# Optimization experiments

Hardware: AMD Instinct MI355X
Metric: run time of the kernel (lower is better)

The kernel has to match this reference:

```python
import jax, jax.numpy as jnp
import numpy as np

NP, NA, H, K, TAU = 4096, 2048, 128, 5, 1.0
NODE_N = {'paper': NP, 'author': NA}
RELS = [('pp', 'paper', 'paper'), ('aa', 'author', 'author'),
        ('pa', 'paper', 'author'), ('ap', 'author', 'paper')]


def setup_inputs():
    key = jax.random.key(0)
    ks = jax.random.split(key, 32)
    f32 = jnp.float32
    def nrm(k, shape, scale=1.0):
        return jax.random.normal(k, shape, f32) * scale
    Epp, Eaa, Epa, Eap = 131072, 65536, 131072, 131072
    inp = {
        'x_paper': nrm(ks[0], (NP, H)),
        'x_author': nrm(ks[1], (NA, H)),
        'ei_pp': jax.random.randint(ks[2], (2, Epp), 0, NP, dtype=jnp.int32),
        'ei_aa': jax.random.randint(ks[3], (2, Eaa), 0, NA, dtype=jnp.int32),
        'ei_pa': jnp.stack([jax.random.randint(ks[4], (Epa,), 0, NP, dtype=jnp.int32),
                            jax.random.randint(ks[5], (Epa,), 0, NA, dtype=jnp.int32)]),
        'ei_ap': jnp.stack([jax.random.randint(ks[6], (Eap,), 0, NA, dtype=jnp.int32),
                            jax.random.randint(ks[7], (Eap,), 0, NP, dtype=jnp.int32)]),
        'batch_paper': jnp.zeros((NP,), jnp.int32),
        'batch_author': jnp.zeros((NA,), jnp.int32),
        'index': 7,
    }
    s = H ** -0.5
    i = 8
    for t in ('paper', 'author'):
        for l in (0, 1):
            inp['Wself_%s%d' % (t, l)] = nrm(ks[i], (H, H), s); i += 1
    for r, _, _ in RELS:
        for l in (0, 1):
            inp['W%s%d' % (r, l)] = nrm(ks[i], (H, H), s); i += 1
    for r in ('pp', 'aa'):
        inp['Wep1_%s' % r] = nrm(ks[i], (2 * H, 256), (2 * H) ** -0.5); i += 1
        inp['bep1_%s' % r] = jnp.zeros((256,), f32)
        inp['Wep2_%s' % r] = nrm(ks[i], (256, 2), 256 ** -0.5); i += 1
        inp['bep2_%s' % r] = jnp.zeros((2,), f32)
    inp['Wc'] = nrm(ks[i], (H, 5), s)
    inp['bc'] = jnp.zeros((5,), f32)
    return inp


def _mean_agg(msg, dst, n):
    s = jax.ops.segment_sum(msg, dst, num_segments=n)
    c = jax.ops.segment_sum(jnp.ones((msg.shape[0], 1), msg.dtype), dst, num_segments=n)
    return s / jnp.maximum(c, 1.0)


def _gnn(x, ei, p, single, edge_attn=None):
    # 2-layer relation-typed mean-aggregation hetero GNN.
    h = dict(x)
    for l in (0, 1):
        nh = {}
        for t in ('paper', 'author'):
            agg = h[t] @ p['Wself_%s%d' % (t, l)]
            for r, s_t, d_t in RELS:
                if d_t != t or (single and s_t != d_t):
                    continue
                src, dst = ei[r][0], ei[r][1]
                msg = h[s_t][src] @ p['W%s%d' % (r, l)]  # [E, H]
                if edge_attn is not None and r in edge_attn:
                    msg = msg * edge_attn[r][:, None]
                agg = agg + _mean_agg(msg, dst, NODE_N[t])
            nh[t] = jax.nn.relu(agg)
        h = nh
    return h


def _edge_pred(h, ei, p, r, t):
    src, dst = ei[r][0], ei[r][1]
    e = jnp.concatenate([h[t][src], h[t][dst]], axis=-1)  # [E, 2H]
    e = jax.nn.relu(e @ p['Wep1_%s' % r] + p['bep1_%s' % r])
    return e @ p['Wep2_%s' % r] + p['bep2_%s' % r]  # [E, 2]


def _gumbel_topk(logits, mask, k, tau, key):
    # Masked straight-through top-k gumbel-softmax (row-wise, hard=True).
    u = jax.random.uniform(key, logits.shape, logits.dtype, 1e-10, 1.0)
    g = -jnp.log(-jnp.log(u))
    y = jnp.where(mask, (logits + g) / tau, -1e9)
    soft = jax.nn.softmax(y, axis=-1)
    _, idx = jax.lax.top_k(soft, k)  # [N, k]
    rows = jnp.arange(logits.shape[0])[:, None]
    hard = jnp.zeros_like(soft).at[rows, idx].set(1.0)
    return hard - jax.lax.stop_gradient(soft) + soft


def _prune(h, ei, p, r, t, n, key):
    pred = _edge_pred(h, ei, p, r, t)[:, 0]
    src, dst = ei[r][0], ei[r][1]
    # sparse_coo_tensor(...).to_dense(): duplicates coalesce by sum
    A = jnp.zeros((n, n), pred.dtype).at[src, dst].add(pred)
    S = _gumbel_topk(A, A > 0, K, TAU, key)
    return S[src, dst]


def _forward(p, ints):
    x = {'paper': p['x_paper'], 'author': p['x_author']}
    ei = {'pp': ints['ei_pp'], 'aa': ints['ei_aa'], 'pa': ints['ei_pa'], 'ap': ints['ei_ap']}
    h1 = _gnn(x, ei, p, single=True)
    kpp, kaa = jax.random.split(jax.random.key(42))
    w_pp = _prune(h1, ei, p, 'pp', 'paper', NP, kpp)
    w_aa = _prune(h1, ei, p, 'aa', 'author', NA, kaa)
    h2 = _gnn(x, ei, p, single=False, edge_attn={'pp': w_pp, 'aa': w_aa})
    pool = h2['paper'][ints['index']].reshape(1, -1)
    y_hat = pool @ p['Wc'] + p['bc']
    return y_hat, w_pp, w_aa


def reference(x_paper, x_author, ei_pp, ei_aa, ei_pa, ei_ap, batch_paper, batch_author, index,
              Wself_paper0, Wself_paper1, Wself_author0, Wself_author1,
              Wpp0, Wpp1, Waa0, Waa1, Wpa0, Wpa1, Wap0, Wap1,
              Wep1_pp, bep1_pp, Wep2_pp, bep2_pp, Wep1_aa, bep1_aa, Wep2_aa, bep2_aa,
              Wc, bc):
    p = dict(x_paper=x_paper, x_author=x_author,
             Wself_paper0=Wself_paper0, Wself_paper1=Wself_paper1,
             Wself_author0=Wself_author0, Wself_author1=Wself_author1,
             Wpp0=Wpp0, Wpp1=Wpp1, Waa0=Waa0, Waa1=Waa1,
             Wpa0=Wpa0, Wpa1=Wpa1, Wap0=Wap0, Wap1=Wap1,
             Wep1_pp=Wep1_pp, bep1_pp=bep1_pp, Wep2_pp=Wep2_pp, bep2_pp=bep2_pp,
             Wep1_aa=Wep1_aa, bep1_aa=bep1_aa, Wep2_aa=Wep2_aa, bep2_aa=bep2_aa,
             Wc=Wc, bc=bc)
    ints = dict(ei_pp=ei_pp, ei_aa=ei_aa, ei_pa=ei_pa, ei_ap=ei_ap, index=index)
    return _forward(p, ints)
```

## Files before the change

### kernel.cpp

```cpp
#include <hip/hip_runtime.h>
#include <stdint.h>


namespace {

constexpr int NPn = 4096;
constexpr int NAn = 2048;
constexpr int Hh  = 128;
constexpr int EPPc = 131072;
constexpr int EAAc = 65536;
constexpr int KSEL = 5;
constexpr int BSLOT = 128;


__host__ __device__ static inline void tf2x32(uint32_t k0, uint32_t k1,
                                              uint32_t& x0, uint32_t& x1) {
  uint32_t ks2 = k0 ^ k1 ^ 0x1BD11BDAu;
  x0 += k0; x1 += k1;
#define TF_R(r) { x0 += x1; x1 = (x1 << (r)) | (x1 >> (32 - (r))); x1 ^= x0; }
  TF_R(13) TF_R(15) TF_R(26) TF_R(6)
  x0 += k1;  x1 += ks2 + 1u;
  TF_R(17) TF_R(29) TF_R(16) TF_R(24)
  x0 += ks2; x1 += k0 + 2u;
  TF_R(13) TF_R(15) TF_R(26) TF_R(6)
  x0 += k0;  x1 += k1 + 3u;
  TF_R(17) TF_R(29) TF_R(16) TF_R(24)
  x0 += k1;  x1 += ks2 + 4u;
  TF_R(13) TF_R(15) TF_R(26) TF_R(6)
  x0 += ks2; x1 += k0 + 5u;
#undef TF_R
}

__global__ __launch_bounds__(256) void scatter_kernel(
    const int* src_pp, const int* dst_pp, const int* src_aa, const int* dst_aa,
    const int* src_pa, const int* dst_pa, const int* src_ap, const int* dst_ap,
    int* cnt, int* entries)
{
  int i = blockIdx.x * 256 + threadIdx.x;
  int key, pl;
  if (i < 131072) {
    int e = i;
    key = 0 + dst_pp[e]; pl = (src_pp[e] << 18) | e;
  } else if (i < 196608) {
    int e = i - 131072;
    key = 4096 + dst_aa[e]; pl = (src_aa[e] << 16) | e;
  } else if (i < 327680) {
    int e = i - 196608;
    key = 6144 + dst_pa[e]; pl = src_pa[e];
  } else if (i < 458752) {
    int e = i - 327680;
    key = 8192 + dst_ap[e]; pl = src_ap[e];
  } else if (i < 589824) {
    int e = i - 458752;
    key = 12288 + src_pp[e]; pl = (dst_pp[e] << 18) | e;
  } else if (i < 655360) {
    int e = i - 589824;
    key = 16384 + src_aa[e]; pl = (dst_aa[e] << 16) | e;
  } else return;
  int pos = atomicAdd(&cnt[key], 1);
  if (pos < BSLOT) entries[key * BSLOT + pos] = pl;
}

struct FDesc {
  const float* gsrc; const float* wArr; int cntOff; int shift;
  float* Mout;
  const float* Aself; const float* W0; const float* W1;
  const float* A2;  const float* W2;
  float* C; int relu;
  const float* WP; float* P1; float* P2;
};
struct FArgs { FDesc d[4]; int bstart[5]; int nd; };

__global__ __launch_bounds__(256) void fused_layer(FArgs fa, const int* __restrict__ cnt,
                                                   const int* __restrict__ entries)
{
  __shared__ __align__(16) float Xs[8][128];
  __shared__ __align__(16) float Ms[8][128];
  __shared__ __align__(16) float Zs[8][128];
  int blk = blockIdx.x, tid = threadIdx.x;
  int di = 0;
  while (di < fa.nd - 1 && blk >= fa.bstart[di + 1]) ++di;
  FDesc D = fa.d[di];
  int node0 = (blk - fa.bstart[di]) * 8;
  {
    int hw = tid >> 5;
    int node = node0 + hw;
    int fl = (tid & 31) << 2;
    int deg = cnt[D.cntOff + node];
    const int* ent = entries + (size_t)(D.cntOff + node) * BSLOT;
    const float* h = D.gsrc;
    int sh = D.shift;
    float ax = 0.f, ay = 0.f, az = 0.f, aw = 0.f;
    if (D.wArr) {
      unsigned mask = (1u << sh) - 1u;
      int k = 0;
      for (; k + 3 < deg; k += 4) {
        unsigned p0 = (unsigned)ent[k], p1 = (unsigned)ent[k + 1];
        unsigned p2 = (unsigned)ent[k + 2], p3 = (unsigned)ent[k + 3];
        float w0 = D.wArr[p0 & mask], w1 = D.wArr[p1 & mask];
        float w2v = D.wArr[p2 & mask], w3 = D.wArr[p3 & mask];
        float4 v0, v1, v2, v3;
        if (w0 != 0.f) v0 = *(const float4*)&h[(size_t)(p0 >> sh) * Hh + fl];
        if (w1 != 0.f) v1 = *(const float4*)&h[(size_t)(p1 >> sh) * Hh + fl];
        if (w2v != 0.f) v2 = *(const float4*)&h[(size_t)(p2 >> sh) * Hh + fl];
        if (w3 != 0.f) v3 = *(const float4*)&h[(size_t)(p3 >> sh) * Hh + fl];
        if (w0 != 0.f) { ax += v0.x; ay += v0.y; az += v0.z; aw += v0.w; }
        if (w1 != 0.f) { ax += v1.x; ay += v1.y; az += v1.z; aw += v1.w; }
        if (w2v != 0.f) { ax += v2.x; ay += v2.y; az += v2.z; aw += v2.w; }
        if (w3 != 0.f) { ax += v3.x; ay += v3.y; az += v3.z; aw += v3.w; }
      }
      for (; k < deg; ++k) {
        unsigned pl = (unsigned)ent[k];
        float wt = D.wArr[pl & mask];
        if (wt != 0.f) {
          float4 v = *(const float4*)&h[(size_t)(pl >> sh) * Hh + fl];
          ax += v.x; ay += v.y; az += v.z; aw += v.w;
        }
      }
    } else {
      int k = 0;
      for (; k + 7 < deg; k += 8) {
        unsigned p0 = (unsigned)ent[k],     p1 = (unsigned)ent[k + 1];
        unsigned p2 = (unsigned)ent[k + 2], p3 = (unsigned)ent[k + 3];
        unsigned p4 = (unsigned)ent[k + 4], p5 = (unsigned)ent[k + 5];
        unsigned p6 = (unsigned)ent[k + 6], p7 = (unsigned)ent[k + 7];
        float4 v0 = *(const float4*)&h[(size_t)(p0 >> sh) * Hh + fl];
        float4 v1 = *(const float4*)&h[(size_t)(p1 >> sh) * Hh + fl];
        float4 v2 = *(const float4*)&h[(size_t)(p2 >> sh) * Hh + fl];
        float4 v3 = *(const float4*)&h[(size_t)(p3 >> sh) * Hh + fl];
        float4 v4 = *(const float4*)&h[(size_t)(p4 >> sh) * Hh + fl];
        float4 v5 = *(const float4*)&h[(size_t)(p5 >> sh) * Hh + fl];
        float4 v6 = *(const float4*)&h[(size_t)(p6 >> sh) * Hh + fl];
        float4 v7 = *(const float4*)&h[(size_t)(p7 >> sh) * Hh + fl];
        ax += v0.x; ay += v0.y; az += v0.z; aw += v0.w;
        ax += v1.x; ay += v1.y; az += v1.z; aw += v1.w;
        ax += v2.x; ay += v2.y; az += v2.z; aw += v2.w;
        ax += v3.x; ay += v3.y; az += v3.z; aw += v3.w;
        ax += v4.x; ay += v4.y; az += v4.z; aw += v4.w;
        ax += v5.x; ay += v5.y; az += v5.z; aw += v5.w;
        ax += v6.x; ay += v6.y; az += v6.z; aw += v6.w;
        ax += v7.x; ay += v7.y; az += v7.z; aw += v7.w;
      }
      for (; k < deg; ++k) {
        unsigned pl = (unsigned)ent[k];
        float4 v = *(const float4*)&h[(size_t)(pl >> sh) * Hh + fl];
        ax += v.x; ay += v.y; az += v.z; aw += v.w;
      }
    }
    float cd = fmaxf((float)deg, 1.0f);
    float4 o; o.x = ax / cd; o.y = ay / cd; o.z = az / cd; o.w = aw / cd;
    if (D.W0 == nullptr) {
      *(float4*)&D.Mout[(size_t)node * Hh + fl] = o;
    } else {
      *(float4*)&Ms[hw][fl] = o;
    }
  }
  if (D.W0 == nullptr) return;
  {
    int rm = tid >> 5, cq = (tid & 31) << 2;
    *(float4*)&Xs[rm][cq] = *(const float4*)&D.Aself[(size_t)(node0 + rm) * 128 + cq];
    if (D.A2)
      *(float4*)&Zs[rm][cq] = *(const float4*)&D.A2[(size_t)(node0 + rm) * 128 + cq];
  }
  __syncthreads();
  int m = tid >> 5, nq = tid & 31;
  float4 accv = {0.f, 0.f, 0.f, 0.f};
  int parts = D.A2 ? 3 : 2;
  for (int p = 0; p < parts; ++p) {
    const float* W = (p == 0) ? D.W0 : (p == 1) ? D.W1 : D.W2;
    const float* Wc_ = W + (nq << 2);
#define KPART(AR)                                                   \
    _Pragma("unroll 2")                                             \
    for (int k = 0; k < 128; k += 4) {                              \
      float4 av = *(const float4*)&AR[m][k];                        \
      float4 w0 = *(const float4*)&Wc_[(size_t)(k + 0) * 128];      \
      float4 w1 = *(const float4*)&Wc_[(size_t)(k + 1) * 128];      \
      float4 w2 = *(const float4*)&Wc_[(size_t)(k + 2) * 128];      \
      float4 w3 = *(const float4*)&Wc_[(size_t)(k + 3) * 128];      \
      accv.x += av.x * w0.x; accv.y += av.x * w0.y;                 \
      accv.z += av.x * w0.z; accv.w += av.x * w0.w;                 \
      accv.x += av.y * w1.x; accv.y += av.y * w1.y;                 \
      accv.z += av.y * w1.z; accv.w += av.y * w1.w;                 \
      accv.x += av.z * w2.x; accv.y += av.z * w2.y;                 \
      accv.z += av.z * w2.z; accv.w += av.z * w2.w;                 \
      accv.x += av.w * w3.x; accv.y += av.w * w3.y;                 \
      accv.z += av.w * w3.z; accv.w += av.w * w3.w;                 \
    }
    if (p == 0) { KPART(Xs) } else if (p == 1) { KPART(Ms) } else { KPART(Zs) }
#undef KPART
  }
  if (D.relu) {
    accv.x = fmaxf(accv.x, 0.f); accv.y = fmaxf(accv.y, 0.f);
    accv.z = fmaxf(accv.z, 0.f); accv.w = fmaxf(accv.w, 0.f);
  }
  if (D.C)
    *(float4*)&D.C[(size_t)(node0 + m) * 128 + (nq << 2)] = accv;
  if (D.WP == nullptr) return;
  __syncthreads();
  *(float4*)&Xs[m][nq << 2] = accv;
  __syncthreads();
  {
    int half = tid >> 7;
    int rg = (tid >> 6) & 1;
    int c0 = (tid & 63) << 2;
    const float* Wb = D.WP + ((size_t)(half ? 128 : 0)) * 256 + c0;
    float4 acc0 = {0,0,0,0}, acc1 = {0,0,0,0}, acc2 = {0,0,0,0}, acc3 = {0,0,0,0};
    for (int k = 0; k < 128; k += 2) {
      float4 w0 = *(const float4*)&Wb[(size_t)k * 256];
      float4 w1 = *(const float4*)&Wb[(size_t)(k + 1) * 256];
      float2 a0 = *(const float2*)&Xs[rg * 4 + 0][k];
      float2 a1 = *(const float2*)&Xs[rg * 4 + 1][k];
      float2 a2 = *(const float2*)&Xs[rg * 4 + 2][k];
      float2 a3 = *(const float2*)&Xs[rg * 4 + 3][k];
      acc0.x += a0.x * w0.x; acc0.y += a0.x * w0.y; acc0.z += a0.x * w0.z; acc0.w += a0.x * w0.w;
      acc0.x += a0.y * w1.x; acc0.y += a0.y * w1.y; acc0.z += a0.y * w1.z; acc0.w += a0.y * w1.w;
      acc1.x += a1.x * w0.x; acc1.y += a1.x * w0.y; acc1.z += a1.x * w0.z; acc1.w += a1.x * w0.w;
      acc1.x += a1.y * w1.x; acc1.y += a1.y * w1.y; acc1.z += a1.y * w1.z; acc1.w += a1.y * w1.w;
      acc2.x += a2.x * w0.x; acc2.y += a2.x * w0.y; acc2.z += a2.x * w0.z; acc2.w += a2.x * w0.w;
      acc2.x += a2.y * w1.x; acc2.y += a2.y * w1.y; acc2.z += a2.y * w1.z; acc2.w += a2.y * w1.w;
      acc3.x += a3.x * w0.x; acc3.y += a3.x * w0.y; acc3.z += a3.x * w0.z; acc3.w += a3.x * w0.w;
      acc3.x += a3.y * w1.x; acc3.y += a3.y * w1.y; acc3.z += a3.y * w1.z; acc3.w += a3.y * w1.w;
    }
    float* Pout = half ? D.P2 : D.P1;
    *(float4*)&Pout[(size_t)(node0 + rg * 4 + 0) * 256 + c0] = acc0;
    *(float4*)&Pout[(size_t)(node0 + rg * 4 + 1) * 256 + c0] = acc1;
    *(float4*)&Pout[(size_t)(node0 + rg * 4 + 2) * 256 + c0] = acc2;
    *(float4*)&Pout[(size_t)(node0 + rg * 4 + 3) * 256 + c0] = acc3;
  }
}

__global__ __launch_bounds__(256) void row_topk(
    const float* __restrict__ P1pp, const float* __restrict__ P2pp,
    const float* __restrict__ b1pp, const float* __restrict__ W2pp,
    const float* __restrict__ b2pp,
    const float* __restrict__ P1aa, const float* __restrict__ P2aa,
    const float* __restrict__ b1aa, const float* __restrict__ W2aa,
    const float* __restrict__ b2aa,
    const int* __restrict__ cnt, const int* __restrict__ entries,
    float* __restrict__ w_pp, float* __restrict__ w_aa,
    uint32_t kpp0, uint32_t kpp1, uint32_t kaa0, uint32_t kaa1)
{
  __shared__ int   dS[4][128];
  __shared__ float pS[4][128];
  __shared__ int   sel5[4][KSEL];
  int blk = blockIdx.x, tid = threadIdx.x;
  int lane = tid & 63, wv = tid >> 6;
  int row, Ncols, shift;
  int co; unsigned mask;
  const float* P1; const float* P2; const float* b1; const float* W2; const float* b2;
  float* wout; uint32_t k0, k1;
  if (blk < NPn / 4) {
    row = blk * 4 + wv; Ncols = NPn; shift = 18; mask = 0x3FFFFu; co = 12288;
    P1 = P1pp; P2 = P2pp; b1 = b1pp; W2 = W2pp; b2 = b2pp;
    wout = w_pp; k0 = kpp0; k1 = kpp1;
  } else {
    row = (blk - NPn / 4) * 4 + wv; Ncols = NAn; shift = 16; mask = 0xFFFFu; co = 16384;
    P1 = P1aa; P2 = P2aa; b1 = b1aa; W2 = W2aa; b2 = b2aa;
    wout = w_aa; k0 = kaa0; k1 = kaa1;
  }
  const int* ent = entries + (size_t)(co + row) * BSLOT;
  int deg = cnt[co + row];
  int j = lane << 2;
  float4 p1v = *(const float4*)&P1[(size_t)row * 256 + j];
  float4 b1v = *(const float4*)&b1[j];
  float wa = W2[(j + 0) * 2], wb = W2[(j + 1) * 2];
  float wc = W2[(j + 2) * 2], wd = W2[(j + 3) * 2];
  float bias2 = b2[0];
  float pa = p1v.x, pb = p1v.y, pc = p1v.z, pd = p1v.w;
  float ba = b1v.x, bb = b1v.y, bc_ = b1v.z, bd = b1v.w;
#define SCORE(q) (fmaxf(pa + q.x + ba, 0.f) * wa + fmaxf(pb + q.y + bb, 0.f) * wb + \
                  fmaxf(pc + q.z + bc_, 0.f) * wc + fmaxf(pd + q.w + bd, 0.f) * wd)
  for (int k = 0; k < deg; k += 8) {
    int n = deg - k; if (n > 8) n = 8;
    unsigned pl0 = (unsigned)ent[k];
    unsigned pl1 = (n > 1) ? (unsigned)ent[k + 1] : pl0;
    unsigned pl2 = (n > 2) ? (unsigned)ent[k + 2] : pl0;
    unsigned pl3 = (n > 3) ? (unsigned)ent[k + 3] : pl0;
    unsigned pl4 = (n > 4) ? (unsigned)ent[k + 4] : pl0;
    unsigned pl5 = (n > 5) ? (unsigned)ent[k + 5] : pl0;
    unsigned pl6 = (n > 6) ? (unsigned)ent[k + 6] : pl0;
    unsigned pl7 = (n > 7) ? (unsigned)ent[k + 7] : pl0;
    int d0 = (int)(pl0 >> shift), d1 = (int)(pl1 >> shift);
    int d2 = (int)(pl2 >> shift), d3 = (int)(pl3 >> shift);
    int d4 = (int)(pl4 >> shift), d5 = (int)(pl5 >> shift);
    int d6 = (int)(pl6 >> shift), d7 = (int)(pl7 >> shift);
    float4 q0 = *(const float4*)&P2[(size_t)d0 * 256 + j];
    float4 q1 = *(const float4*)&P2[(size_t)d1 * 256 + j];
    float4 q2 = *(const float4*)&P2[(size_t)d2 * 256 + j];
    float4 q3 = *(const float4*)&P2[(size_t)d3 * 256 + j];
    float4 q4 = *(const float4*)&P2[(size_t)d4 * 256 + j];
    float4 q5 = *(const float4*)&P2[(size_t)d5 * 256 + j];
    float4 q6 = *(const float4*)&P2[(size_t)d6 * 256 + j];
    float4 q7 = *(const float4*)&P2[(size_t)d7 * 256 + j];
    float s0 = SCORE(q0), s1 = SCORE(q1), s2 = SCORE(q2), s3 = SCORE(q3);
    float s4 = SCORE(q4), s5 = SCORE(q5), s6 = SCORE(q6), s7 = SCORE(q7);
    for (int off = 32; off; off >>= 1) {
      s0 += __shfl_down(s0, off);
      s1 += __shfl_down(s1, off);
      s2 += __shfl_down(s2, off);
      s3 += __shfl_down(s3, off);
      s4 += __shfl_down(s4, off);
      s5 += __shfl_down(s5, off);
      s6 += __shfl_down(s6, off);
      s7 += __shfl_down(s7, off);
    }
    if (lane == 0) {
      dS[wv][k] = d0; pS[wv][k] = s0 + bias2;
      if (n > 1) { dS[wv][k + 1] = d1; pS[wv][k + 1] = s1 + bias2; }
      if (n > 2) { dS[wv][k + 2] = d2; pS[wv][k + 2] = s2 + bias2; }
      if (n > 3) { dS[wv][k + 3] = d3; pS[wv][k + 3] = s3 + bias2; }
      if (n > 4) { dS[wv][k + 4] = d4; pS[wv][k + 4] = s4 + bias2; }
      if (n > 5) { dS[wv][k + 5] = d5; pS[wv][k + 5] = s5 + bias2; }
      if (n > 6) { dS[wv][k + 6] = d6; pS[wv][k + 6] = s6 + bias2; }
      if (n > 7) { dS[wv][k + 7] = d7; pS[wv][k + 7] = s7 + bias2; }
    }
  }
#undef SCORE
  __syncthreads();
  if (deg > 0) {
    int   e0 = (lane < deg) ? dS[wv][lane] : -1;
    float q0v = (lane < deg) ? pS[wv][lane] : 0.f;
    bool  two = (deg > 64);
    int   e1 = -1; float q1v = 0.f;
    if (two && 64 + lane < deg) { e1 = dS[wv][64 + lane]; q1v = pS[wv][64 + lane]; }
    float a0 = 0.f, a1 = 0.f;
    bool lead0 = (e0 >= 0), lead1 = (e1 >= 0);
    for (int j2 = 0; j2 < deg; ++j2) {
      int bj; float bp;
      if (j2 < 64) { bj = __shfl(e0, j2); bp = __shfl(q0v, j2); }
      else         { bj = __shfl(e1, j2 - 64); bp = __shfl(q1v, j2 - 64); }
      if (e0 >= 0 && bj == e0) { a0 += bp; if (j2 < lane) lead0 = false; }
      if (e1 >= 0 && bj == e1) { a1 += bp; if (j2 < 64 + lane) lead1 = false; }
    }
    uint32_t rowbase = (uint32_t)row * (uint32_t)Ncols;
    float y0 = -1e9f, y1 = -1e9f;
    bool c0 = lead0 && (a0 > 0.f);
    if (c0) {
      uint32_t x0 = 0u, x1 = rowbase + (uint32_t)e0;
      tf2x32(k0, k1, x0, x1);
      uint32_t bits = x0 ^ x1;
      float fv = __uint_as_float((bits >> 9) | 0x3f800000u) - 1.0f;
      float u = fmaxf(1e-10f, fv + 1e-10f);
      y0 = a0 + (-logf(-logf(u)));
    }
    bool c1 = lead1 && (a1 > 0.f);
    if (c1) {
      uint32_t x0 = 0u, x1 = rowbase + (uint32_t)e1;
      tf2x32(k0, k1, x0, x1);
      uint32_t bits = x0 ^ x1;
      float fv = __uint_as_float((bits >> 9) | 0x3f800000u) - 1.0f;
      float u = fmaxf(1e-10f, fv + 1e-10f);
      y1 = a1 + (-logf(-logf(u)));
    }
    int cnt2 = __popcll(__ballot(c0)) + __popcll(__ballot(c1));
    int nsel = cnt2 < KSEL ? cnt2 : KSEL;
    for (int it = 0; it < nsel; ++it) {
      float best; int bc;
      if (y1 > y0 || (y1 == y0 && (unsigned)e1 < (unsigned)e0)) { best = y1; bc = e1; }
      else { best = y0; bc = e0; }
      for (int mm = 32; mm; mm >>= 1) {
        float ov = __shfl_xor(best, mm); int oc = __shfl_xor(bc, mm);
        if (ov > best || (ov == best && (unsigned)oc < (unsigned)bc)) { best = ov; bc = oc; }
      }
      if (lane == 0) sel5[wv][it] = bc;
      if (e0 == bc) y0 = -3.0e38f;
      if (e1 == bc) y1 = -3.0e38f;
    }
    if (nsel < KSEL && lane == 0) {
      int c = 0;
      for (int it = nsel; it < KSEL; ++it) {
        for (;;) {
          bool used = false;
          for (int q = 0; q < it; ++q) used |= (sel5[wv][q] == c);
          if (!used) break;
          ++c;
        }
        sel5[wv][it] = c++;
      }
    }
  }
  __syncthreads();
  for (int k = lane; k < deg; k += 64) {
    unsigned pl = (unsigned)ent[k];
    int d = (int)(pl >> shift);
    int e = (int)(pl & mask);
    float v = 0.f;
#pragma unroll
    for (int q = 0; q < KSEL; ++q) v = (sel5[wv][q] == d) ? 1.f : v;
    wout[e] = v;
  }
}

__global__ __launch_bounds__(128) void final_kernel(
    const float* __restrict__ hp, const float* __restrict__ ha,
    const int* __restrict__ idxPtr, const float* __restrict__ wpp,
    const int* __restrict__ cnt, const int* __restrict__ entries,
    const float* __restrict__ Wself, const float* __restrict__ Wpp,
    const float* __restrict__ Wap,
    const float* __restrict__ Wc, const float* __restrict__ bc,
    float* __restrict__ out)
{
  __shared__ float selfr[128], mpp[128], mapr[128], t[128];
  int tid = threadIdx.x;
  int idx = idxPtr[0];
  selfr[tid] = hp[(size_t)idx * 128 + tid];
  {
    int deg = cnt[idx];
    const int* ent = entries + (size_t)idx * BSLOT;
    float acc = 0.f;
    for (int k = 0; k < deg; ++k) {
      unsigned pl = (unsigned)ent[k];
      int s = (int)(pl >> 18);
      int e = (int)(pl & 0x3FFFFu);
      acc += wpp[e] * hp[(size_t)s * 128 + tid];
    }
    mpp[tid] = acc / fmaxf((float)deg, 1.0f);
  }
  {
    int deg = cnt[8192 + idx];
    const int* ent = entries + (size_t)(8192 + idx) * BSLOT;
    float acc = 0.f;
    for (int k = 0; k < deg; ++k) {
      int s = ent[k];
      acc += ha[(size_t)s * 128 + tid];
    }
    mapr[tid] = acc / fmaxf((float)deg, 1.0f);
  }
  __syncthreads();
  float s = 0.f;
  for (int m = 0; m < 128; ++m) {
    s += selfr[m] * Wself[m * 128 + tid] + mpp[m] * Wpp[m * 128 + tid] +
         mapr[m] * Wap[m * 128 + tid];
  }
  t[tid] = fmaxf(s, 0.f);
  __syncthreads();
  if (tid < 5) {
    float y = bc[tid];
    for (int k = 0; k < 128; ++k) y += t[k] * Wc[k * 5 + tid];
    out[tid] = y;
  }
}

}

extern "C" void kernel_launch(void* const* d_in, const int* in_sizes, int n_in,
                              void* d_out, int out_size, void* d_ws, size_t ws_size,
                              hipStream_t stream)
{
  (void)in_sizes; (void)n_in; (void)out_size; (void)ws_size;
  const float* x_p = (const float*)d_in[0];
  const float* x_a = (const float*)d_in[1];
  const int* ei_pp = (const int*)d_in[2];
  const int* ei_aa = (const int*)d_in[3];
  const int* ei_pa = (const int*)d_in[4];
  const int* ei_ap = (const int*)d_in[5];
  const int* idxPtr = (const int*)d_in[8];
  const float* Wself_p0 = (const float*)d_in[9];
  const float* Wself_p1 = (const float*)d_in[10];
  const float* Wself_a0 = (const float*)d_in[11];
  const float* Wself_a1 = (const float*)d_in[12];
  const float* Wpp0 = (const float*)d_in[13]; const float* Wpp1 = (const float*)d_in[14];
  const float* Waa0 = (const float*)d_in[15]; const float* Waa1 = (const float*)d_in[16];
  const float* Wpa0 = (const float*)d_in[17];
  const float* Wap0 = (const float*)d_in[19]; const float* Wap1 = (const float*)d_in[20];
  const float* Wep1_pp = (const float*)d_in[21]; const float* bep1_pp = (const float*)d_in[22];
  const float* Wep2_pp = (const float*)d_in[23]; const float* bep2_pp = (const float*)d_in[24];
  const float* Wep1_aa = (const float*)d_in[25]; const float* bep1_aa = (const float*)d_in[26];
  const float* Wep2_aa = (const float*)d_in[27]; const float* bep2_aa = (const float*)d_in[28];
  const float* Wc = (const float*)d_in[29]; const float* bc = (const float*)d_in[30];

  float* out = (float*)d_out;
  float* w_pp_out = out + 5;
  float* w_aa_out = out + 5 + EPPc;

  const int* src_pp = ei_pp;  const int* dst_pp = ei_pp + EPPc;
  const int* src_aa = ei_aa;  const int* dst_aa = ei_aa + EAAc;
  const int* src_pa = ei_pa;  const int* dst_pa = ei_pa + 131072;
  const int* src_ap = ei_ap;  const int* dst_ap = ei_ap + 131072;

  char* p = (char*)d_ws;
  auto alloc = [&](size_t bytes) -> void* {
    void* r = (void*)p;
    p += (bytes + 255) & ~(size_t)255;
    return r;
  };
  int* cnt     = (int*)alloc(18432 * sizeof(int));
  int* entries = (int*)alloc((size_t)18432 * BSLOT * sizeof(int));
  float* Map  = (float*)alloc((size_t)NPn * Hh * sizeof(float));
  float* Mpa  = (float*)alloc((size_t)NAn * Hh * sizeof(float));
  float* h1p0 = (float*)alloc((size_t)NPn * Hh * sizeof(float));
  float* h1a0 = (float*)alloc((size_t)NAn * Hh * sizeof(float));
  float* h2p0 = (float*)alloc((size_t)NPn * Hh * sizeof(float));
  float* h2a0 = (float*)alloc((size_t)NAn * Hh * sizeof(float));
  float* P1pp = (float*)alloc((size_t)NPn * 256 * sizeof(float));
  float* P2pp = (float*)alloc((size_t)NPn * 256 * sizeof(float));
  float* P1aa = (float*)alloc((size_t)NAn * 256 * sizeof(float));
  float* P2aa = (float*)alloc((size_t)NAn * 256 * sizeof(float));

  const int CO_PPD = 0, CO_AAD = 4096, CO_PAD = 6144, CO_APD = 8192;

  hipMemsetAsync(cnt, 0, 18432 * sizeof(int), stream);
  scatter_kernel<<<2560, 256, 0, stream>>>(src_pp, dst_pp, src_aa, dst_aa,
                                           src_pa, dst_pa, src_ap, dst_ap,
                                           cnt, entries);

  {
    FArgs fa{};
    fa.d[0] = {x_p, nullptr, CO_PPD, 18, nullptr,
               x_p, Wself_p0, Wpp0, nullptr, nullptr, h1p0, 1,
               nullptr, nullptr, nullptr};
    fa.d[1] = {x_a, nullptr, CO_AAD, 16, nullptr,
               x_a, Wself_a0, Waa0, nullptr, nullptr, h1a0, 1,
               nullptr, nullptr, nullptr};
    fa.d[2] = {x_a, nullptr, CO_APD, 0, Map,
               nullptr, nullptr, nullptr, nullptr, nullptr, nullptr, 0,
               nullptr, nullptr, nullptr};
    fa.d[3] = {x_p, nullptr, CO_PAD, 0, Mpa,
               nullptr, nullptr, nullptr, nullptr, nullptr, nullptr, 0,
               nullptr, nullptr, nullptr};
    fa.bstart[0] = 0; fa.bstart[1] = 512; fa.bstart[2] = 768;
    fa.bstart[3] = 1280; fa.bstart[4] = 1536; fa.nd = 4;
    fused_layer<<<1536, 256, 0, stream>>>(fa, cnt, entries);
  }

  {
    FArgs fa{};
    fa.d[0] = {h1p0, nullptr, CO_PPD, 18, nullptr,
               h1p0, Wself_p1, Wpp1, nullptr, nullptr, nullptr, 1,
               Wep1_pp, P1pp, P2pp};
    fa.d[1] = {h1a0, nullptr, CO_AAD, 16, nullptr,
               h1a0, Wself_a1, Waa1, nullptr, nullptr, nullptr, 1,
               Wep1_aa, P1aa, P2aa};
    fa.bstart[0] = 0; fa.bstart[1] = 512; fa.bstart[2] = 768; fa.nd = 2;
    fused_layer<<<768, 256, 0, stream>>>(fa, cnt, entries);
  }

  uint32_t kpp0, kpp1, kaa0, kaa1;
  { uint32_t a0 = 0, a1 = 0; tf2x32(0u, 42u, a0, a1); kpp0 = a0; kpp1 = a1; }
  { uint32_t a0 = 0, a1 = 1; tf2x32(0u, 42u, a0, a1); kaa0 = a0; kaa1 = a1; }

  row_topk<<<(NPn + NAn) / 4, 256, 0, stream>>>(P1pp, P2pp, bep1_pp, Wep2_pp, bep2_pp,
                                                P1aa, P2aa, bep1_aa, Wep2_aa, bep2_aa,
                                                cnt, entries, w_pp_out, w_aa_out,
                                                kpp0, kpp1, kaa0, kaa1);

  {
    FArgs fa{};
    fa.d[0] = {x_p, w_pp_out, CO_PPD, 18, nullptr,
               x_p, Wself_p0, Wpp0, Map, Wap0, h2p0, 1,
               nullptr, nullptr, nullptr};
    fa.d[1] = {x_a, w_aa_out, CO_AAD, 16, nullptr,
               x_a, Wself_a0, Waa0, Mpa, Wpa0, h2a0, 1,
               nullptr, nullptr, nullptr};
    fa.bstart[0] = 0; fa.bstart[1] = 512; fa.bstart[2] = 768; fa.nd = 2;
    fused_layer<<<768, 256, 0, stream>>>(fa, cnt, entries);
  }

  final_kernel<<<1, 128, 0, stream>>>(h2p0, h2a0, idxPtr, w_pp_out,
                                      cnt, entries,
                                      Wself_p1, Wpp1, Wap1, Wc, bc, out);
}
```

Measured before the change: 357.7 us.

## Stage weight matrices through shared memory in double-buffered 32-row chunks

The fused layer's dense matmul now loads W0/W1/W2 cooperatively into a 32x128 shared-memory tile, one chunk at a time. The next chunk is prefetched into registers while the current one is consumed. Before, each thread read weights straight from global memory with strided float4 loads, and the 8 warps in a block redundantly fetched the same rows. The change adds 16KB of LDS per block and two barriers per chunk, which may lower occupancy and add sync overhead given only 8 rows per block.

```diff
diff --git a/kernel.cpp b/kernel.cpp
--- a/kernel.cpp
+++ b/kernel.cpp
@@ -77,6 +77,7 @@
   __shared__ __align__(16) float Xs[8][128];
   __shared__ __align__(16) float Ms[8][128];
   __shared__ __align__(16) float Zs[8][128];
+  __shared__ __align__(16) float Ws[32][128];
   int blk = blockIdx.x, tid = threadIdx.x;
   int di = 0;
   while (di < fa.nd - 1 && blk >= fa.bstart[di + 1]) ++di;
@@ -162,32 +163,55 @@
     if (D.A2)
       *(float4*)&Zs[rm][cq] = *(const float4*)&D.A2[(size_t)(node0 + rm) * 128 + cq];
   }
-  __syncthreads();
   int m = tid >> 5, nq = tid & 31;
+  int r = tid >> 3, f = (tid & 7) << 4;
   float4 accv = {0.f, 0.f, 0.f, 0.f};
   int parts = D.A2 ? 3 : 2;
-  for (int p = 0; p < parts; ++p) {
-    const float* W = (p == 0) ? D.W0 : (p == 1) ? D.W1 : D.W2;
-    const float* Wc_ = W + (nq << 2);
-#define KPART(AR)                                                   \
-    _Pragma("unroll 2")                                             \
-    for (int k = 0; k < 128; k += 4) {                              \
-      float4 av = *(const float4*)&AR[m][k];                        \
-      float4 w0 = *(const float4*)&Wc_[(size_t)(k + 0) * 128];      \
-      float4 w1 = *(const float4*)&Wc_[(size_t)(k + 1) * 128];      \
-      float4 w2 = *(const float4*)&Wc_[(size_t)(k + 2) * 128];      \
-      float4 w3 = *(const float4*)&Wc_[(size_t)(k + 3) * 128];      \
-      accv.x += av.x * w0.x; accv.y += av.x * w0.y;                 \
-      accv.z += av.x * w0.z; accv.w += av.x * w0.w;                 \
-      accv.x += av.y * w1.x; accv.y += av.y * w1.y;                 \
-      accv.z += av.y * w1.z; accv.w += av.y * w1.w;                 \
-      accv.x += av.z * w2.x; accv.y += av.z * w2.y;                 \
-      accv.z += av.z * w2.z; accv.w += av.z * w2.w;                 \
-      accv.x += av.w * w3.x; accv.y += av.w * w3.y;                 \
-      accv.z += av.w * w3.z; accv.w += av.w * w3.w;                 \
-    }
-    if (p == 0) { KPART(Xs) } else if (p == 1) { KPART(Ms) } else { KPART(Zs) }
-#undef KPART
+  int T = parts * 4;
+  float4 g0, g1, g2, g3;
+  {
+    const float* srcp = &D.W0[(size_t)r * 128 + f];
+    g0 = *(const float4*)&srcp[0];
+    g1 = *(const float4*)&srcp[4];
+    g2 = *(const float4*)&srcp[8];
+    g3 = *(const float4*)&srcp[12];
+  }
+  for (int t = 0; t < T; ++t) {
+    __syncthreads();
+    *(float4*)&Ws[r][f]      = g0;
+    *(float4*)&Ws[r][f + 4]  = g1;
+    *(float4*)&Ws[r][f + 8]  = g2;
+    *(float4*)&Ws[r][f + 12] = g3;
+    if (t + 1 < T) {
+      int p2 = (t + 1) >> 2, ci = (t + 1) & 3;
+      const float* Wn = (p2 == 0) ? D.W0 : (p2 == 1) ? D.W1 : D.W2;
+      const float* srcp = &Wn[(size_t)(ci * 32 + r) * 128 + f];
+      g0 = *(const float4*)&srcp[0];
+      g1 = *(const float4*)&srcp[4];
+      g2 = *(const float4*)&srcp[8];
+      g3 = *(const float4*)&srcp[12];
+    }
+    __syncthreads();
+    int p = t >> 2, c = t & 3;
+#define KCHUNK(AR)                                              \
+    _Pragma("unroll")                                           \
+    for (int k4 = 0; k4 < 32; k4 += 4) {                        \
+      float4 av = *(const float4*)&AR[m][c * 32 + k4];          \
+      float4 w0 = *(const float4*)&Ws[k4 + 0][nq << 2];         \
+      float4 w1 = *(const float4*)&Ws[k4 + 1][nq << 2];         \
+      float4 w2v = *(const float4*)&Ws[k4 + 2][nq << 2];        \
+      float4 w3 = *(const float4*)&Ws[k4 + 3][nq << 2];         \
+      accv.x += av.x * w0.x; accv.y += av.x * w0.y;             \
+      accv.z += av.x * w0.z; accv.w += av.x * w0.w;             \
+      accv.x += av.y * w1.x; accv.y += av.y * w1.y;             \
+      accv.z += av.y * w1.z; accv.w += av.y * w1.w;             \
+      accv.x += av.z * w2v.x; accv.y += av.z * w2v.y;           \
+      accv.z += av.z * w2v.z; accv.w += av.z * w2v.w;           \
+      accv.x += av.w * w3.x; accv.y += av.w * w3.y;             \
+      accv.z += av.w * w3.z; accv.w += av.w * w3.w;             \
+    }
+    if (p == 0) { KCHUNK(Xs) } else if (p == 1) { KCHUNK(Ms) } else { KCHUNK(Zs) }
+#undef KCHUNK
   }
   if (D.relu) {
     accv.x = fmaxf(accv.x, 0.f); accv.y = fmaxf(accv.y, 0.f);
```

Result: faster. 322.5 us (-9.9%).
